# Kernel tuning notes

Measured on AMD Instinct MI355X. Metric: run time of the kernel, lower is better.

The kernel has to match this reference:

```python
import jax, jax.numpy as jnp
import numpy as np

BATCH, TOP_K, MAX_LEN, EMB_DIM = 8, 64, 256, 768


def setup_inputs() -> dict:
    key = jax.random.key(0)
    context = jax.random.normal(key, (BATCH, TOP_K, 2, MAX_LEN, EMB_DIM), dtype=jnp.float32)
    return {"context": context}


def reference(context):
    # context: [B, K, 2, L, D]; slice 0 = context tokens, slice 1 = entity tokens
    ctx = context[:, :, 0, :, :]   # [B, K, L, D]
    ent = context[:, :, 1, :, :]   # [B, K, L, D]
    # similarity: for each context token, score against every entity token
    sim = jnp.einsum("bkld,bkmd->bklm", ctx, ent)  # [B, K, L, L]
    idx = jnp.argmax(sim, axis=-1)                 # [B, K, L] hard attention index
    # gather best-matching entity token per context token
    sel = jnp.take_along_axis(ent, idx[..., None], axis=2)  # [B, K, L, D]
    # dot product per token then sum over tokens (sum-of-max score)
    out = jnp.sum(ctx * sel, axis=(-1, -2))        # [B, K]
    return out
```

## Files before the change

kernel.cpp:

```cpp
#include <hip/hip_runtime.h>


#define MAXLEN 256
#define EMB 768
#define BK 64
#define NSTEP 12
#define LSTRIDE 72

typedef __attribute__((ext_vector_type(4))) float f32x4;
typedef __attribute__((ext_vector_type(8))) short short8;
typedef __bf16 bf16x8 __attribute__((ext_vector_type(8)));

__device__ inline unsigned int pack2bf(float a, float b) {
  unsigned int ua = __builtin_bit_cast(unsigned int, a);
  unsigned int ub = __builtin_bit_cast(unsigned int, b);
  ua = (ua + (0x7fffu + ((ua >> 16) & 1u))) >> 16;
  ub = (ub + (0x7fffu + ((ub >> 16) & 1u))) & 0xffff0000u;
  return ua | ub;
}

__device__ inline uint2 pack4bf(float4 v) {
  uint2 r;
  r.x = pack2bf(v.x, v.y);
  r.y = pack2bf(v.z, v.w);
  return r;
}

__device__ inline bf16x8 pack8bf(float4 a, float4 b) {
  union { unsigned int u[4]; bf16x8 v; } r;
  r.u[0] = pack2bf(a.x, a.y);
  r.u[1] = pack2bf(a.z, a.w);
  r.u[2] = pack2bf(b.x, b.y);
  r.u[3] = pack2bf(b.z, b.w);
  return r.v;
}

__global__ __launch_bounds__(512, 2) void som_rowmax_kernel(
    const float* __restrict__ ctx_all, float* __restrict__ out) {
  __shared__ __align__(16) short lsB[2][MAXLEN][LSTRIDE];
  __shared__ float red[8];

  const int t    = threadIdx.x;
  const int w    = t >> 6;
  const int lane = t & 63;
  const int qw   = lane >> 4;
  const int lr   = lane & 15;

  const size_t p = blockIdx.x;
  const float* ctx = ctx_all + p * (size_t)(2 * MAXLEN * EMB);
  const float* ent = ctx + (size_t)(MAXLEN * EMB);

  const int srow = t >> 4;
  const int scol = (t & 15) * 4;
  const float* gB = ent + (size_t)srow * EMB + scol;

  const int lt0 = 2 * w, lt1 = 2 * w + 1;
  const float* gA0 = ctx + (size_t)(lt0 * 16 + lr) * EMB + qw * 8;
  const float* gA1 = ctx + (size_t)(lt1 * 16 + lr) * EMB + qw * 8;

  f32x4 acc[2][16];
#pragma unroll
  for (int h = 0; h < 2; ++h)
#pragma unroll
    for (int mt = 0; mt < 16; ++mt)
      acc[h][mt] = (f32x4){0.f, 0.f, 0.f, 0.f};

  float4 rb[8];
  float4 raA[8];
  bf16x8 afr[2][2];

  auto issueB = [&](int s) {
#pragma unroll
    for (int r = 0; r < 8; ++r)
      rb[r] = *(const float4*)(gB + (size_t)r * (32 * EMB) + s * BK);
  };
  auto commitB = [&](int buf) {
#pragma unroll
    for (int r = 0; r < 8; ++r) {
      const int row = r * 32 + srow;
      *(uint2*)&lsB[buf][row][scol] = pack4bf(rb[r]);
    }
  };
  auto issueA = [&](int s) {
#pragma unroll
    for (int kh = 0; kh < 2; ++kh)
#pragma unroll
      for (int half = 0; half < 2; ++half) {
        raA[0 * 4 + kh * 2 + half] = *(const float4*)(gA0 + s * BK + kh * 32 + half * 4);
        raA[1 * 4 + kh * 2 + half] = *(const float4*)(gA1 + s * BK + kh * 32 + half * 4);
      }
  };
  auto packA = [&]() {
#pragma unroll
    for (int tile = 0; tile < 2; ++tile)
#pragma unroll
      for (int kh = 0; kh < 2; ++kh)
        afr[tile][kh] = pack8bf(raA[tile * 4 + kh * 2 + 0], raA[tile * 4 + kh * 2 + 1]);
  };
  auto mfmaStep = [&](int buf) {
#pragma unroll
    for (int kh = 0; kh < 2; ++kh) {
      const int kq = kh * 32 + qw * 8;
#pragma unroll
      for (int mt = 0; mt < 16; ++mt) {
        bf16x8 bfr = __builtin_bit_cast(bf16x8, *(const short8*)&lsB[buf][mt * 16 + lr][kq]);
        acc[0][mt] = __builtin_amdgcn_mfma_f32_16x16x32_bf16(afr[0][kh], bfr, acc[0][mt], 0, 0, 0);
        acc[1][mt] = __builtin_amdgcn_mfma_f32_16x16x32_bf16(afr[1][kh], bfr, acc[1][mt], 0, 0, 0);
      }
    }
  };
  auto barrier = [&]() {
    asm volatile("s_waitcnt lgkmcnt(0)" ::: "memory");
    __builtin_amdgcn_sched_barrier(0);
    __builtin_amdgcn_s_barrier();
    __builtin_amdgcn_sched_barrier(0);
  };

  issueB(0);
  issueA(0);
  commitB(0);
  issueB(1);
  packA();
  barrier();

  for (int s = 0; s < NSTEP - 2; ++s) {
    issueA(s + 1);
    commitB((s + 1) & 1);
    issueB(s + 2);
    mfmaStep(s & 1);
    packA();
    barrier();
  }
  issueA(NSTEP - 1);
  commitB((NSTEP - 1) & 1);
  mfmaStep((NSTEP - 2) & 1);
  packA();
  barrier();
  mfmaStep((NSTEP - 1) & 1);

  float s = 0.f;
#pragma unroll
  for (int h = 0; h < 2; ++h) {
#pragma unroll
    for (int i = 0; i < 4; ++i) {
      float m = acc[h][0][i];
#pragma unroll
      for (int mt = 1; mt < 16; ++mt) m = fmaxf(m, acc[h][mt][i]);
#pragma unroll
      for (int d = 1; d < 16; d <<= 1) m = fmaxf(m, __shfl_xor(m, d, 64));
      s += m;
    }
  }
  s += __shfl_xor(s, 16, 64);
  s += __shfl_xor(s, 32, 64);

  if (lane == 0) red[w] = s;
  __syncthreads();
  if (t == 0) {
    float tot = 0.f;
#pragma unroll
    for (int i = 0; i < 8; ++i) tot += red[i];
    out[p] = tot;
  }
}

extern "C" void kernel_launch(void* const* d_in, const int* in_sizes, int n_in,
                              void* d_out, int out_size, void* d_ws, size_t ws_size,
                              hipStream_t stream) {
  const float* ctx_all = (const float*)d_in[0];
  float* out = (float*)d_out;
  som_rowmax_kernel<<<dim3(512), dim3(512), 0, stream>>>(ctx_all, out);
}
```

Baseline: 150.6 us.

## Use single-buffered LDS with 128-wide K steps and builtin bf16 conversion

Doubles the K chunk per step from 64 to 128, halving the number of steps and barriers. It replaces the double-buffered LDS with one buffer, reorders the pipeline into compute, barrier, reload, barrier, and swaps the manual round-to-nearest bf16 packing for compiler bf16 casts that may map to hardware convert instructions. The tradeoff is an extra barrier per step, no overlap of LDS writes with MFMA, and more registers held in flight (16 float4 each for A and B), which may threaten two-block occupancy.

Result: slower. 239.4 us (+59.0%).

```diff
diff --git a/kernel.cpp b/kernel.cpp
--- a/kernel.cpp
+++ b/kernel.cpp
@@ -3,41 +3,32 @@
 
 #define MAXLEN 256
 #define EMB 768
-#define BK 64
-#define NSTEP 12
-#define LSTRIDE 72
+#define BK 128
+#define NSTEP 6
+#define LSTRIDE 138
 
 typedef __attribute__((ext_vector_type(4))) float f32x4;
 typedef __attribute__((ext_vector_type(8))) short short8;
 typedef __bf16 bf16x8 __attribute__((ext_vector_type(8)));
+typedef __bf16 bf16x4 __attribute__((ext_vector_type(4)));
 
-__device__ inline unsigned int pack2bf(float a, float b) {
-  unsigned int ua = __builtin_bit_cast(unsigned int, a);
-  unsigned int ub = __builtin_bit_cast(unsigned int, b);
-  ua = (ua + (0x7fffu + ((ua >> 16) & 1u))) >> 16;
-  ub = (ub + (0x7fffu + ((ub >> 16) & 1u))) & 0xffff0000u;
-  return ua | ub;
-}
-
-__device__ inline uint2 pack4bf(float4 v) {
-  uint2 r;
-  r.x = pack2bf(v.x, v.y);
-  r.y = pack2bf(v.z, v.w);
+__device__ inline bf16x8 cvt8(float4 a, float4 b) {
+  bf16x8 r;
+  r[0] = (__bf16)a.x; r[1] = (__bf16)a.y; r[2] = (__bf16)a.z; r[3] = (__bf16)a.w;
+  r[4] = (__bf16)b.x; r[5] = (__bf16)b.y; r[6] = (__bf16)b.z; r[7] = (__bf16)b.w;
   return r;
 }
 
-__device__ inline bf16x8 pack8bf(float4 a, float4 b) {
-  union { unsigned int u[4]; bf16x8 v; } r;
-  r.u[0] = pack2bf(a.x, a.y);
-  r.u[1] = pack2bf(a.z, a.w);
-  r.u[2] = pack2bf(b.x, b.y);
-  r.u[3] = pack2bf(b.z, b.w);
-  return r.v;
+__device__ inline uint2 cvt4u(float4 v) {
+  union { uint2 u; bf16x4 h; } r;
+  r.h[0] = (__bf16)v.x; r.h[1] = (__bf16)v.y;
+  r.h[2] = (__bf16)v.z; r.h[3] = (__bf16)v.w;
+  return r.u;
 }
 
 __global__ __launch_bounds__(512, 2) void som_rowmax_kernel(
     const float* __restrict__ ctx_all, float* __restrict__ out) {
-  __shared__ __align__(16) short lsB[2][MAXLEN][LSTRIDE];
+  __shared__ __align__(16) short lsB[MAXLEN][LSTRIDE];
   __shared__ float red[8];
 
   const int t    = threadIdx.x;
@@ -50,13 +41,12 @@
   const float* ctx = ctx_all + p * (size_t)(2 * MAXLEN * EMB);
   const float* ent = ctx + (size_t)(MAXLEN * EMB);
 
-  const int srow = t >> 4;
-  const int scol = (t & 15) * 4;
+  const int srow = t >> 5;
+  const int scol = (t & 31) * 4;
   const float* gB = ent + (size_t)srow * EMB + scol;
 
-  const int lt0 = 2 * w, lt1 = 2 * w + 1;
-  const float* gA0 = ctx + (size_t)(lt0 * 16 + lr) * EMB + qw * 8;
-  const float* gA1 = ctx + (size_t)(lt1 * 16 + lr) * EMB + qw * 8;
+  const float* gA0 = ctx + (size_t)(32 * w + lr) * EMB + qw * 8;
+  const float* gA1 = ctx + (size_t)(32 * w + 16 + lr) * EMB + qw * 8;
 
   f32x4 acc[2][16];
 #pragma unroll
@@ -65,45 +55,47 @@
     for (int mt = 0; mt < 16; ++mt)
       acc[h][mt] = (f32x4){0.f, 0.f, 0.f, 0.f};
 
-  float4 rb[8];
-  float4 raA[8];
-  bf16x8 afr[2][2];
+  float4 rb[16];
+  float4 raA[16];
+  bf16x8 afr[2][4];
 
-  auto issueB = [&](int s) {
+  auto issueB = [&](int s, int h) {
 #pragma unroll
     for (int r = 0; r < 8; ++r)
-      rb[r] = *(const float4*)(gB + (size_t)r * (32 * EMB) + s * BK);
+      rb[h * 8 + r] = *(const float4*)(gB + (size_t)(h * 8 + r) * (16 * EMB) + s * BK);
   };
-  auto commitB = [&](int buf) {
+  auto commitB = [&]() {
 #pragma unroll
-    for (int r = 0; r < 8; ++r) {
-      const int row = r * 32 + srow;
-      *(uint2*)&lsB[buf][row][scol] = pack4bf(rb[r]);
+    for (int r = 0; r < 16; ++r) {
+      const int row = r * 16 + srow;
+      *(uint2*)&lsB[row][scol] = cvt4u(rb[r]);
     }
   };
-  auto issueA = [&](int s) {
+  auto issueA = [&](int s, int h) {
 #pragma unroll
-    for (int kh = 0; kh < 2; ++kh)
+    for (int kk = 0; kk < 2; ++kk) {
+      const int kh = 2 * h + kk;
 #pragma unroll
       for (int half = 0; half < 2; ++half) {
-        raA[0 * 4 + kh * 2 + half] = *(const float4*)(gA0 + s * BK + kh * 32 + half * 4);
-        raA[1 * 4 + kh * 2 + half] = *(const float4*)(gA1 + s * BK + kh * 32 + half * 4);
+        raA[0 * 8 + kh * 2 + half] = *(const float4*)(gA0 + s * BK + kh * 32 + half * 4);
+        raA[1 * 8 + kh * 2 + half] = *(const float4*)(gA1 + s * BK + kh * 32 + half * 4);
       }
+    }
   };
   auto packA = [&]() {
 #pragma unroll
     for (int tile = 0; tile < 2; ++tile)
 #pragma unroll
-      for (int kh = 0; kh < 2; ++kh)
-        afr[tile][kh] = pack8bf(raA[tile * 4 + kh * 2 + 0], raA[tile * 4 + kh * 2 + 1]);
+      for (int kh = 0; kh < 4; ++kh)
+        afr[tile][kh] = cvt8(raA[tile * 8 + kh * 2 + 0], raA[tile * 8 + kh * 2 + 1]);
   };
-  auto mfmaStep = [&](int buf) {
+  auto mfmaStep = [&]() {
 #pragma unroll
-    for (int kh = 0; kh < 2; ++kh) {
+    for (int kh = 0; kh < 4; ++kh) {
       const int kq = kh * 32 + qw * 8;
 #pragma unroll
       for (int mt = 0; mt < 16; ++mt) {
-        bf16x8 bfr = __builtin_bit_cast(bf16x8, *(const short8*)&lsB[buf][mt * 16 + lr][kq]);
+        bf16x8 bfr = __builtin_bit_cast(bf16x8, *(const short8*)&lsB[mt * 16 + lr][kq]);
         acc[0][mt] = __builtin_amdgcn_mfma_f32_16x16x32_bf16(afr[0][kh], bfr, acc[0][mt], 0, 0, 0);
         acc[1][mt] = __builtin_amdgcn_mfma_f32_16x16x32_bf16(afr[1][kh], bfr, acc[1][mt], 0, 0, 0);
       }
@@ -116,27 +108,28 @@
     __builtin_amdgcn_sched_barrier(0);
   };
 
-  issueB(0);
-  issueA(0);
-  commitB(0);
-  issueB(1);
+  issueB(0, 0);
+  issueB(0, 1);
+  commitB();
+  issueA(0, 0);
+  issueA(0, 1);
+  issueB(1, 0);
+  issueB(1, 1);
   packA();
   barrier();
 
-  for (int s = 0; s < NSTEP - 2; ++s) {
-    issueA(s + 1);
-    commitB((s + 1) & 1);
-    issueB(s + 2);
-    mfmaStep(s & 1);
+  for (int s = 0; s < NSTEP - 1; ++s) {
+    mfmaStep();
+    barrier();
+    issueA(s + 1, 0);
+    commitB();
+    issueA(s + 1, 1);
+    if (s + 2 < NSTEP) issueB(s + 2, 0);
     packA();
+    if (s + 2 < NSTEP) issueB(s + 2, 1);
     barrier();
   }
-  issueA(NSTEP - 1);
-  commitB((NSTEP - 1) & 1);
-  mfmaStep((NSTEP - 2) & 1);
-  packA();
-  barrier();
-  mfmaStep((NSTEP - 1) & 1);
+  mfmaStep();
 
   float s = 0.f;
 #pragma unroll
```
